# Kernel optimization log

Hardware: AMD Instinct MI355X
Metric: run time of the kernel (lower is better)

Reference implementation:

```python
import jax, jax.numpy as jnp
import numpy as np

N = 100000   # nodes
E = 3200000  # edges
G = 64       # graphs in batch
F_IN = 128   # num_features
H = 8        # hidden per TAGConv (hard-coded in module)
K = 3        # TAGConv hops (PyG default)
L = 3        # num_layers


def setup_inputs() -> dict:
    key = jax.random.key(0)
    ks = jax.random.split(key, 8)
    x = jax.random.normal(ks[0], (N, F_IN), dtype=jnp.float32)
    edge_index = jax.random.randint(ks[1], (2, E), 0, N, dtype=jnp.int32)
    batch = jnp.sort(jax.random.randint(ks[2], (N,), 0, G, dtype=jnp.int32))
    edge_weight = jax.random.uniform(ks[3], (E,), dtype=jnp.float32)
    W1 = jax.random.normal(ks[4], ((K + 1) * F_IN, H), dtype=jnp.float32) * 0.05
    W2 = jax.random.normal(ks[5], ((K + 1) * H, H), dtype=jnp.float32) * 0.1
    W3 = jax.random.normal(ks[6], ((K + 1) * H, H), dtype=jnp.float32) * 0.1
    fcW = jax.random.normal(ks[7], (2 * L * H, 2), dtype=jnp.float32) * 0.1
    return {
        'x': x, 'edge_index': edge_index, 'batch': batch,
        'edge_weight': edge_weight,
        'W1': W1, 'b1': jnp.zeros((H,), jnp.float32),
        'W2': W2, 'b2': jnp.zeros((H,), jnp.float32),
        'W3': W3, 'b3': jnp.zeros((H,), jnp.float32),
        'fcW': fcW, 'fcb': jnp.zeros((2,), jnp.float32),
    }


def _tag_conv(h, src, dst, norm, W, b):
    # TAGConv: concat [h, T h, T^2 h, T^3 h] then one linear (== sum of per-hop linears)
    xs = [h]
    for _ in range(K):
        h = jax.ops.segment_sum(h[src] * norm[:, None], dst, num_segments=N)
        xs.append(h)
    return jnp.concatenate(xs, axis=-1) @ W + b


def reference(x, edge_index, batch, edge_weight, W1, b1, W2, b2, W3, b3, fcW, fcb):
    src, dst = edge_index[0], edge_index[1]
    # GCN symmetric normalization, no self loops (PyG TAGConv default)
    deg = jax.ops.segment_sum(edge_weight, dst, num_segments=N)
    safe = jnp.where(deg > 0, deg, 1.0)
    dis = jnp.where(deg > 0, jax.lax.rsqrt(safe), 0.0)
    norm = dis[src] * edge_weight * dis[dst]  # [E]

    h = jax.nn.relu(_tag_conv(x, src, dst, norm, W1, b1))
    xs = [h]
    for (W, b) in ((W2, b2), (W3, b3)):
        h = jax.nn.relu(_tag_conv(h, src, dst, norm, W, b))
        xs.append(h)
    jk = jnp.concatenate(xs, axis=-1)  # [N, L*H] = [N, 24]

    # global max pool + global mean pool per graph
    gmax = jax.ops.segment_max(jk, batch, num_segments=G)
    gmax = jnp.where(jnp.isfinite(gmax), gmax, 0.0)
    gsum = jax.ops.segment_sum(jk, batch, num_segments=G)
    cnt = jax.ops.segment_sum(jnp.ones((N,), jk.dtype), batch, num_segments=G)
    gmean = gsum / jnp.maximum(cnt, 1.0)[:, None]
    pooled = jnp.concatenate([gmax, gmean], axis=-1)  # [G, 48]
    return pooled @ fcW + fcb  # [G, 2]
```

## Files before the change

kernel.cpp:

```cpp
#include <hip/hip_runtime.h>

static inline int div_up(int a, int b){ return (a + b - 1) / b; }

constexpr int FIN = 128;
constexpr unsigned long long DEG_MASK = ((unsigned long long)1 << 48) - 1;


__global__ __launch_bounds__(256) void count_deg_k(const int* __restrict__ dst,
    const float* __restrict__ w, unsigned long long* __restrict__ packed,
    unsigned short* __restrict__ ie, int E)
{
    int e = blockIdx.x * 256 + threadIdx.x;
    if (e >= E) return;
    int d = dst[e];
    unsigned long long add = ((unsigned long long)1 << 48)
                           | (unsigned long long)(w[e] * 4294967296.0f);
    unsigned long long old = atomicAdd(&packed[d], add);
    ie[e] = (unsigned short)(old >> 48);
}

__global__ __launch_bounds__(256) void scan_sum_k(const unsigned long long* __restrict__ packed,
    int* __restrict__ bsum, int n)
{
    __shared__ int lds[256];
    int t = threadIdx.x;
    int base = blockIdx.x * 1024 + t * 4;
    int s = 0;
    #pragma unroll
    for (int i = 0; i < 4; ++i) if (base + i < n) s += (int)(packed[base + i] >> 48);
    lds[t] = s; __syncthreads();
    for (int o = 128; o > 0; o >>= 1){
        if (t < o) lds[t] += lds[t + o];
        __syncthreads();
    }
    if (t == 0) bsum[blockIdx.x] = lds[0];
}

__global__ __launch_bounds__(256) void scan_block_k(int* __restrict__ bsum, int nb,
    int* __restrict__ rowptr, int n, int Etot)
{
    __shared__ int lds[256];
    int t = threadIdx.x;
    int v = (t < nb) ? bsum[t] : 0;
    lds[t] = v; __syncthreads();
    for (int o = 1; o < 256; o <<= 1){
        int add = (t >= o) ? lds[t - o] : 0;
        __syncthreads();
        lds[t] += add;
        __syncthreads();
    }
    if (t < nb) bsum[t] = lds[t] - v;
    if (t == 0) rowptr[n] = Etot;
}

__global__ __launch_bounds__(256) void scan_apply_k(const unsigned long long* __restrict__ packed,
    const int* __restrict__ bsum, int* __restrict__ rowptr, float* __restrict__ dis, int n)
{
    __shared__ int lds[256];
    int t = threadIdx.x;
    int base = blockIdx.x * 1024 + t * 4;
    int v[4]; int ts = 0;
    unsigned long long pk[4];
    #pragma unroll
    for (int i = 0; i < 4; ++i){
        pk[i] = (base + i < n) ? packed[base + i] : 0ull;
        v[i] = (int)(pk[i] >> 48); ts += v[i];
    }
    lds[t] = ts; __syncthreads();
    for (int o = 1; o < 256; o <<= 1){
        int add = (t >= o) ? lds[t - o] : 0;
        __syncthreads();
        lds[t] += add;
        __syncthreads();
    }
    int pre = lds[t] - ts + bsum[blockIdx.x];
    #pragma unroll
    for (int i = 0; i < 4; ++i){
        if (base + i < n){
            rowptr[base + i] = pre;
            float d = (float)(pk[i] & DEG_MASK) * (1.0f / 4294967296.0f);
            dis[base + i] = d > 0.f ? rsqrtf(d) : 0.f;
        }
        pre += v[i];
    }
}

__global__ __launch_bounds__(256) void scatter_k(const int* __restrict__ src,
    const int* __restrict__ dst, const float* __restrict__ w,
    const float* __restrict__ dis, const int* __restrict__ rowptr,
    const unsigned short* __restrict__ ie, int2* __restrict__ edges, int E)
{
    int e = blockIdx.x * 256 + threadIdx.x;
    if (e >= E) return;
    int s = src[e], d = dst[e];
    float nm = dis[s] * w[e] * dis[d];
    int pos = rowptr[d] + (int)ie[e];
    edges[pos] = make_int2(s, __float_as_int(nm));
}


__global__ __launch_bounds__(256) void gemm1_k(const float* __restrict__ x,
    const float* __restrict__ W, float* __restrict__ z, int n)
{
    int node = blockIdx.x * 256 + threadIdx.x;
    if (node >= n) return;
    const float4* xr = (const float4*)(x + (size_t)node * FIN);
    float acc[32];
    #pragma unroll
    for (int o = 0; o < 32; ++o) acc[o] = 0.f;
    #pragma unroll 2
    for (int fc = 0; fc < FIN / 4; ++fc){
        float4 xv = xr[fc];
        #pragma unroll
        for (int jj = 0; jj < 4; ++jj){
            float xs = jj == 0 ? xv.x : jj == 1 ? xv.y : jj == 2 ? xv.z : xv.w;
            int f = fc * 4 + jj;
            #pragma unroll
            for (int k = 0; k < 4; ++k)
                #pragma unroll
                for (int h = 0; h < 8; ++h)
                    acc[k * 8 + h] = fmaf(xs, W[((size_t)(k * FIN + f)) * 8 + h], acc[k * 8 + h]);
        }
    }
    float4* zr = (float4*)(z + (size_t)node * 32);
    #pragma unroll
    for (int q = 0; q < 8; ++q)
        zr[q] = make_float4(acc[q*4+0], acc[q*4+1], acc[q*4+2], acc[q*4+3]);
}

__global__ __launch_bounds__(256) void gemm_small_k(const float* __restrict__ hin,
    const float* __restrict__ W, float* __restrict__ z, int n)
{
    int node = blockIdx.x * 256 + threadIdx.x;
    if (node >= n) return;
    const float4* hr = (const float4*)(hin + (size_t)node * 8);
    float4 p0 = hr[0], p1 = hr[1];
    float hv[8] = {p0.x, p0.y, p0.z, p0.w, p1.x, p1.y, p1.z, p1.w};
    float acc[32];
    #pragma unroll
    for (int o = 0; o < 32; ++o) acc[o] = 0.f;
    #pragma unroll
    for (int f = 0; f < 8; ++f)
        #pragma unroll
        for (int k = 0; k < 4; ++k)
            #pragma unroll
            for (int h = 0; h < 8; ++h)
                acc[k * 8 + h] = fmaf(hv[f], W[(k * 8 + f) * 8 + h], acc[k * 8 + h]);
    float4* zr = (float4*)(z + (size_t)node * 32);
    #pragma unroll
    for (int q = 0; q < 8; ++q)
        zr[q] = make_float4(acc[q*4+0], acc[q*4+1], acc[q*4+2], acc[q*4+3]);
}


template<bool RELU, bool GEMM>
__global__ __launch_bounds__(256) void prop_k(const int2* __restrict__ edges,
    const int* __restrict__ rowptr, const float* __restrict__ uin, int instride,
    const float* __restrict__ addv, const float* __restrict__ bias,
    float* __restrict__ uout, const float* __restrict__ Wn, float* __restrict__ zout, int n)
{
    int t = blockIdx.x * 256 + threadIdx.x;
    int node = t >> 3, g = t & 7;
    if (node >= n) return;
    int r0 = rowptr[node], r1 = rowptr[node + 1];
    float acc = 0.f;
    int j = r0;
    for (; j + 4 <= r1; j += 4){
        int2 e0 = edges[j], e1 = edges[j+1], e2 = edges[j+2], e3 = edges[j+3];
        float a0 = uin[(size_t)e0.x * instride + g];
        float a1 = uin[(size_t)e1.x * instride + g];
        float a2 = uin[(size_t)e2.x * instride + g];
        float a3 = uin[(size_t)e3.x * instride + g];
        acc = fmaf(__int_as_float(e0.y), a0, acc);
        acc = fmaf(__int_as_float(e1.y), a1, acc);
        acc = fmaf(__int_as_float(e2.y), a2, acc);
        acc = fmaf(__int_as_float(e3.y), a3, acc);
    }
    for (; j < r1; ++j){
        int2 e0 = edges[j];
        acc = fmaf(__int_as_float(e0.y), uin[(size_t)e0.x * instride + g], acc);
    }
    float v = addv[(size_t)node * 32 + g] + acc;
    if (RELU) v = fmaxf(v + bias[g], 0.f);
    uout[(size_t)node * 8 + g] = v;
    if (GEMM){
        int lane = threadIdx.x & 63;
        int gbase = lane & ~7;
        float hrow[8];
        #pragma unroll
        for (int f = 0; f < 8; ++f) hrow[f] = __shfl(v, gbase + f);
        float zv[4];
        #pragma unroll
        for (int q = 0; q < 4; ++q){
            int o = g * 4 + q;
            int k = o >> 3, h = o & 7;
            float s = 0.f;
            #pragma unroll
            for (int f = 0; f < 8; ++f)
                s = fmaf(hrow[f], Wn[(k * 8 + f) * 8 + h], s);
            zv[q] = s;
        }
        *(float4*)(zout + (size_t)node * 32 + g * 4) = make_float4(zv[0], zv[1], zv[2], zv[3]);
    }
}


__global__ __launch_bounds__(256) void pool_k(const float* __restrict__ h1,
    const float* __restrict__ h2, const float* __restrict__ h3,
    const int* __restrict__ batch, unsigned* __restrict__ gmaxb,
    float* __restrict__ gsum, int* __restrict__ gcnt, int n)
{
    int t = blockIdx.x * 256 + threadIdx.x;
    int lane = threadIdx.x & 63;
    bool valid = (t < n);
    int b = valid ? batch[t] : -1;
    float v[24];
    #pragma unroll
    for (int q = 0; q < 24; ++q) v[q] = 0.f;
    if (valid){
        const float4* p1 = (const float4*)(h1 + (size_t)t * 8);
        const float4* p2 = (const float4*)(h2 + (size_t)t * 8);
        const float4* p3 = (const float4*)(h3 + (size_t)t * 8);
        float4 a0 = p1[0], a1 = p1[1], c0 = p2[0], c1 = p2[1], d0 = p3[0], d1 = p3[1];
        v[0]=a0.x; v[1]=a0.y; v[2]=a0.z; v[3]=a0.w; v[4]=a1.x; v[5]=a1.y; v[6]=a1.z; v[7]=a1.w;
        v[8]=c0.x; v[9]=c0.y; v[10]=c0.z; v[11]=c0.w; v[12]=c1.x; v[13]=c1.y; v[14]=c1.z; v[15]=c1.w;
        v[16]=d0.x; v[17]=d0.y; v[18]=d0.z; v[19]=d0.w; v[20]=d1.x; v[21]=d1.y; v[22]=d1.z; v[23]=d1.w;
    }
    int bl0 = __shfl(b, 0);
    bool uni = __all(b == bl0);
    if (uni){
        if (bl0 >= 0){
            #pragma unroll
            for (int q = 0; q < 24; ++q){
                float s = v[q], m = v[q];
                #pragma unroll
                for (int o = 1; o < 64; o <<= 1){
                    s += __shfl_xor(s, o);
                    m = fmaxf(m, __shfl_xor(m, o));
                }
                if (lane == 0){
                    atomicAdd(&gsum[bl0 * 24 + q], s);
                    atomicMax(&gmaxb[bl0 * 24 + q], __float_as_uint(m));
                }
            }
            if (lane == 0) atomicAdd(&gcnt[bl0], 64);
        }
    } else if (valid){
        #pragma unroll
        for (int q = 0; q < 24; ++q){
            atomicAdd(&gsum[b * 24 + q], v[q]);
            atomicMax(&gmaxb[b * 24 + q], __float_as_uint(v[q]));
        }
        atomicAdd(&gcnt[b], 1);
    }
}

__global__ __launch_bounds__(64) void fc_k(const unsigned* __restrict__ gmaxb,
    const float* __restrict__ gsum, const int* __restrict__ gcnt,
    const float* __restrict__ fcW, const float* __restrict__ fcb,
    float* __restrict__ out, int G)
{
    int g = threadIdx.x;
    if (g >= G) return;
    float pooled[48];
    #pragma unroll
    for (int q = 0; q < 24; ++q) pooled[q] = __uint_as_float(gmaxb[g * 24 + q]);
    float c = (float)gcnt[g];
    if (c < 1.f) c = 1.f;
    float inv = 1.f / c;
    #pragma unroll
    for (int q = 0; q < 24; ++q) pooled[24 + q] = gsum[g * 24 + q] * inv;
    float o0 = fcb[0], o1 = fcb[1];
    #pragma unroll
    for (int j = 0; j < 48; ++j){
        o0 = fmaf(pooled[j], fcW[j * 2 + 0], o0);
        o1 = fmaf(pooled[j], fcW[j * 2 + 1], o1);
    }
    out[g * 2 + 0] = o0;
    out[g * 2 + 1] = o1;
}


extern "C" void kernel_launch(void* const* d_in, const int* in_sizes, int n_in,
                              void* d_out, int out_size, void* d_ws, size_t ws_size,
                              hipStream_t stream)
{
    const float* x    = (const float*)d_in[0];
    const int*   ei   = (const int*)d_in[1];
    const int*   batch= (const int*)d_in[2];
    const float* w    = (const float*)d_in[3];
    const float* W1   = (const float*)d_in[4];
    const float* b1   = (const float*)d_in[5];
    const float* W2   = (const float*)d_in[6];
    const float* b2   = (const float*)d_in[7];
    const float* W3   = (const float*)d_in[8];
    const float* b3   = (const float*)d_in[9];
    const float* fcW  = (const float*)d_in[10];
    const float* fcb  = (const float*)d_in[11];
    float* out = (float*)d_out;

    const int N = in_sizes[2];
    const int E = in_sizes[3];
    const int G = out_size / 2;
    const int* src = ei;
    const int* dst = ei + E;

    char* base = (char*)d_ws;
    size_t off = 0;
    auto alloc = [&](size_t bytes) -> char* {
        char* r = base + off;
        off += (bytes + 255) & ~(size_t)255;
        return r;
    };
    unsigned long long* packed = (unsigned long long*)alloc((size_t)N * 8);
    unsigned* gmaxb  = (unsigned*)alloc((size_t)G * 24 * 4);
    float*    gsum   = (float*)   alloc((size_t)G * 24 * 4);
    int*      gcnt   = (int*)     alloc((size_t)G * 4);
    size_t zero_bytes = off;
    float*    dis    = (float*)   alloc((size_t)N * 4);
    unsigned short* ie = (unsigned short*)alloc((size_t)E * 2);
    int*      rowptr = (int*)     alloc((size_t)(N + 1) * 4);
    int*      bsum   = (int*)     alloc(256 * 4);
    int2*     edges  = (int2*)    alloc((size_t)E * 8);
    float*    zA     = (float*)   alloc((size_t)N * 32 * 4);
    float*    u0     = (float*)   alloc((size_t)N * 8 * 4);
    float*    u1     = (float*)   alloc((size_t)N * 8 * 4);
    float*    h1     = (float*)   alloc((size_t)N * 8 * 4);
    float*    h2     = (float*)   alloc((size_t)N * 8 * 4);
    float*    h3     = (float*)   alloc((size_t)N * 8 * 4);
    float*    zB     = (float*)   alloc((size_t)N * 32 * 4);
    bool fused = (off <= ws_size);
    if (!fused) zB = zA;

    hipMemsetAsync(d_ws, 0, zero_bytes, stream);

    dim3 blk(256);
    count_deg_k<<<div_up(E, 256), blk, 0, stream>>>(dst, w, packed, ie, E);
    int nb = div_up(N, 1024);
    scan_sum_k  <<<nb, blk, 0, stream>>>(packed, bsum, N);
    scan_block_k<<<1,  blk, 0, stream>>>(bsum, nb, rowptr, N, E);
    scan_apply_k<<<nb, blk, 0, stream>>>(packed, bsum, rowptr, dis, N);
    scatter_k<<<div_up(E, 256), blk, 0, stream>>>(src, dst, w, dis, rowptr, ie, edges, E);

    gemm1_k<<<div_up(N, 256), blk, 0, stream>>>(x, W1, zA, N);

    int pb = div_up(N * 8, 256);
    prop_k<false,false><<<pb, blk, 0, stream>>>(edges, rowptr, zA + 24, 32, zA + 16, nullptr, u0, nullptr, nullptr, N);
    prop_k<false,false><<<pb, blk, 0, stream>>>(edges, rowptr, u0, 8, zA + 8, nullptr, u1, nullptr, nullptr, N);
    if (fused){
        prop_k<true,true ><<<pb, blk, 0, stream>>>(edges, rowptr, u1, 8, zA, b1, h1, W2, zB, N);
    } else {
        prop_k<true,false><<<pb, blk, 0, stream>>>(edges, rowptr, u1, 8, zA, b1, h1, nullptr, nullptr, N);
        gemm_small_k<<<div_up(N, 256), blk, 0, stream>>>(h1, W2, zB, N);
    }
    prop_k<false,false><<<pb, blk, 0, stream>>>(edges, rowptr, zB + 24, 32, zB + 16, nullptr, u0, nullptr, nullptr, N);
    prop_k<false,false><<<pb, blk, 0, stream>>>(edges, rowptr, u0, 8, zB + 8, nullptr, u1, nullptr, nullptr, N);
    if (fused){
        prop_k<true,true ><<<pb, blk, 0, stream>>>(edges, rowptr, u1, 8, zB, b2, h2, W3, zA, N);
    } else {
        prop_k<true,false><<<pb, blk, 0, stream>>>(edges, rowptr, u1, 8, zB, b2, h2, nullptr, nullptr, N);
        gemm_small_k<<<div_up(N, 256), blk, 0, stream>>>(h2, W3, zA, N);
    }
    prop_k<false,false><<<pb, blk, 0, stream>>>(edges, rowptr, zA + 24, 32, zA + 16, nullptr, u0, nullptr, nullptr, N);
    prop_k<false,false><<<pb, blk, 0, stream>>>(edges, rowptr, u0, 8, zA + 8, nullptr, u1, nullptr, nullptr, N);
    prop_k<true,false><<<pb, blk, 0, stream>>>(edges, rowptr, u1, 8, zA, b3, h3, nullptr, nullptr, N);

    pool_k<<<div_up(N, 256), blk, 0, stream>>>(h1, h2, h3, batch, gmaxb, gsum, gcnt, N);
    fc_k<<<1, 64, 0, stream>>>(gmaxb, gsum, gcnt, fcW, fcb, out, G);
}
```

Measured before the change: 860.3 us.

## Split per-hop projections into separate arrays and fuse gemm1 into degree counting

Measured after the change: 772.1 us. 1.11x faster.

```diff
diff --git a/kernel.cpp b/kernel.cpp
--- a/kernel.cpp
+++ b/kernel.cpp
@@ -6,17 +6,50 @@
 constexpr unsigned long long DEG_MASK = ((unsigned long long)1 << 48) - 1;
 
 
-__global__ __launch_bounds__(256) void count_deg_k(const int* __restrict__ dst,
-    const float* __restrict__ w, unsigned long long* __restrict__ packed,
-    unsigned short* __restrict__ ie, int E)
-{
-    int e = blockIdx.x * 256 + threadIdx.x;
-    if (e >= E) return;
-    int d = dst[e];
-    unsigned long long add = ((unsigned long long)1 << 48)
-                           | (unsigned long long)(w[e] * 4294967296.0f);
-    unsigned long long old = atomicAdd(&packed[d], add);
-    ie[e] = (unsigned short)(old >> 48);
+__global__ __launch_bounds__(256) void count_gemm1_k(
+    const int* __restrict__ dst, const float* __restrict__ w,
+    unsigned long long* __restrict__ packed, unsigned short* __restrict__ ie, int E, int Eb,
+    const float* __restrict__ x, const float* __restrict__ W,
+    float* __restrict__ z0, float* __restrict__ z1,
+    float* __restrict__ z2, float* __restrict__ z3, int n)
+{
+    if (blockIdx.x < (unsigned)Eb){
+        int e = blockIdx.x * 256 + threadIdx.x;
+        if (e >= E) return;
+        int d = dst[e];
+        unsigned long long add = ((unsigned long long)1 << 48)
+                               | (unsigned long long)(w[e] * 4294967296.0f);
+        unsigned long long old = atomicAdd(&packed[d], add);
+        ie[e] = (unsigned short)(old >> 48);
+    } else {
+        int node = (blockIdx.x - Eb) * 256 + threadIdx.x;
+        if (node >= n) return;
+        const float4* xr = (const float4*)(x + (size_t)node * FIN);
+        float acc[32];
+        #pragma unroll
+        for (int o = 0; o < 32; ++o) acc[o] = 0.f;
+        #pragma unroll 2
+        for (int fc = 0; fc < FIN / 4; ++fc){
+            float4 xv = xr[fc];
+            #pragma unroll
+            for (int jj = 0; jj < 4; ++jj){
+                float xs = jj == 0 ? xv.x : jj == 1 ? xv.y : jj == 2 ? xv.z : xv.w;
+                int f = fc * 4 + jj;
+                #pragma unroll
+                for (int k = 0; k < 4; ++k)
+                    #pragma unroll
+                    for (int h = 0; h < 8; ++h)
+                        acc[k * 8 + h] = fmaf(xs, W[((size_t)(k * FIN + f)) * 8 + h], acc[k * 8 + h]);
+            }
+        }
+        float* zp[4] = {z0, z1, z2, z3};
+        #pragma unroll
+        for (int k = 0; k < 4; ++k){
+            float4* zr = (float4*)(zp[k] + (size_t)node * 8);
+            zr[0] = make_float4(acc[k*8+0], acc[k*8+1], acc[k*8+2], acc[k*8+3]);
+            zr[1] = make_float4(acc[k*8+4], acc[k*8+5], acc[k*8+6], acc[k*8+7]);
+        }
+    }
 }
 
 __global__ __launch_bounds__(256) void scan_sum_k(const unsigned long long* __restrict__ packed,
@@ -99,37 +132,9 @@
 }
 
 
-__global__ __launch_bounds__(256) void gemm1_k(const float* __restrict__ x,
-    const float* __restrict__ W, float* __restrict__ z, int n)
-{
-    int node = blockIdx.x * 256 + threadIdx.x;
-    if (node >= n) return;
-    const float4* xr = (const float4*)(x + (size_t)node * FIN);
-    float acc[32];
-    #pragma unroll
-    for (int o = 0; o < 32; ++o) acc[o] = 0.f;
-    #pragma unroll 2
-    for (int fc = 0; fc < FIN / 4; ++fc){
-        float4 xv = xr[fc];
-        #pragma unroll
-        for (int jj = 0; jj < 4; ++jj){
-            float xs = jj == 0 ? xv.x : jj == 1 ? xv.y : jj == 2 ? xv.z : xv.w;
-            int f = fc * 4 + jj;
-            #pragma unroll
-            for (int k = 0; k < 4; ++k)
-                #pragma unroll
-                for (int h = 0; h < 8; ++h)
-                    acc[k * 8 + h] = fmaf(xs, W[((size_t)(k * FIN + f)) * 8 + h], acc[k * 8 + h]);
-        }
-    }
-    float4* zr = (float4*)(z + (size_t)node * 32);
-    #pragma unroll
-    for (int q = 0; q < 8; ++q)
-        zr[q] = make_float4(acc[q*4+0], acc[q*4+1], acc[q*4+2], acc[q*4+3]);
-}
-
 __global__ __launch_bounds__(256) void gemm_small_k(const float* __restrict__ hin,
-    const float* __restrict__ W, float* __restrict__ z, int n)
+    const float* __restrict__ W, float* __restrict__ z0, float* __restrict__ z1,
+    float* __restrict__ z2, float* __restrict__ z3, int n)
 {
     int node = blockIdx.x * 256 + threadIdx.x;
     if (node >= n) return;
@@ -146,18 +151,23 @@
             #pragma unroll
             for (int h = 0; h < 8; ++h)
                 acc[k * 8 + h] = fmaf(hv[f], W[(k * 8 + f) * 8 + h], acc[k * 8 + h]);
-    float4* zr = (float4*)(z + (size_t)node * 32);
-    #pragma unroll
-    for (int q = 0; q < 8; ++q)
-        zr[q] = make_float4(acc[q*4+0], acc[q*4+1], acc[q*4+2], acc[q*4+3]);
+    float* zp[4] = {z0, z1, z2, z3};
+    #pragma unroll
+    for (int k = 0; k < 4; ++k){
+        float4* zr = (float4*)(zp[k] + (size_t)node * 8);
+        zr[0] = make_float4(acc[k*8+0], acc[k*8+1], acc[k*8+2], acc[k*8+3]);
+        zr[1] = make_float4(acc[k*8+4], acc[k*8+5], acc[k*8+6], acc[k*8+7]);
+    }
 }
 
 
 template<bool RELU, bool GEMM>
 __global__ __launch_bounds__(256) void prop_k(const int2* __restrict__ edges,
-    const int* __restrict__ rowptr, const float* __restrict__ uin, int instride,
+    const int* __restrict__ rowptr, const float* __restrict__ uin,
     const float* __restrict__ addv, const float* __restrict__ bias,
-    float* __restrict__ uout, const float* __restrict__ Wn, float* __restrict__ zout, int n)
+    float* __restrict__ uout, const float* __restrict__ Wn,
+    float* __restrict__ zo0, float* __restrict__ zo1,
+    float* __restrict__ zo2, float* __restrict__ zo3, int n)
 {
     int t = blockIdx.x * 256 + threadIdx.x;
     int node = t >> 3, g = t & 7;
@@ -167,10 +177,10 @@
     int j = r0;
     for (; j + 4 <= r1; j += 4){
         int2 e0 = edges[j], e1 = edges[j+1], e2 = edges[j+2], e3 = edges[j+3];
-        float a0 = uin[(size_t)e0.x * instride + g];
-        float a1 = uin[(size_t)e1.x * instride + g];
-        float a2 = uin[(size_t)e2.x * instride + g];
-        float a3 = uin[(size_t)e3.x * instride + g];
+        float a0 = uin[(size_t)e0.x * 8 + g];
+        float a1 = uin[(size_t)e1.x * 8 + g];
+        float a2 = uin[(size_t)e2.x * 8 + g];
+        float a3 = uin[(size_t)e3.x * 8 + g];
         acc = fmaf(__int_as_float(e0.y), a0, acc);
         acc = fmaf(__int_as_float(e1.y), a1, acc);
         acc = fmaf(__int_as_float(e2.y), a2, acc);
@@ -178,9 +188,9 @@
     }
     for (; j < r1; ++j){
         int2 e0 = edges[j];
-        acc = fmaf(__int_as_float(e0.y), uin[(size_t)e0.x * instride + g], acc);
-    }
-    float v = addv[(size_t)node * 32 + g] + acc;
+        acc = fmaf(__int_as_float(e0.y), uin[(size_t)e0.x * 8 + g], acc);
+    }
+    float v = addv[(size_t)node * 8 + g] + acc;
     if (RELU) v = fmaxf(v + bias[g], 0.f);
     uout[(size_t)node * 8 + g] = v;
     if (GEMM){
@@ -189,18 +199,19 @@
         float hrow[8];
         #pragma unroll
         for (int f = 0; f < 8; ++f) hrow[f] = __shfl(v, gbase + f);
+        int k = g >> 1;
         float zv[4];
         #pragma unroll
         for (int q = 0; q < 4; ++q){
-            int o = g * 4 + q;
-            int k = o >> 3, h = o & 7;
+            int h = (g & 1) * 4 + q;
             float s = 0.f;
             #pragma unroll
             for (int f = 0; f < 8; ++f)
                 s = fmaf(hrow[f], Wn[(k * 8 + f) * 8 + h], s);
             zv[q] = s;
         }
-        *(float4*)(zout + (size_t)node * 32 + g * 4) = make_float4(zv[0], zv[1], zv[2], zv[3]);
+        float* zp = (k == 0) ? zo0 : (k == 1) ? zo1 : (k == 2) ? zo2 : zo3;
+        *(float4*)(zp + (size_t)node * 8 + (g & 1) * 4) = make_float4(zv[0], zv[1], zv[2], zv[3]);
     }
 }
 
@@ -322,48 +333,49 @@
     int*      rowptr = (int*)     alloc((size_t)(N + 1) * 4);
     int*      bsum   = (int*)     alloc(256 * 4);
     int2*     edges  = (int2*)    alloc((size_t)E * 8);
-    float*    zA     = (float*)   alloc((size_t)N * 32 * 4);
+    float*    zA[4], *zB[4];
+    for (int k = 0; k < 4; ++k) zA[k] = (float*)alloc((size_t)N * 8 * 4);
     float*    u0     = (float*)   alloc((size_t)N * 8 * 4);
     float*    u1     = (float*)   alloc((size_t)N * 8 * 4);
     float*    h1     = (float*)   alloc((size_t)N * 8 * 4);
     float*    h2     = (float*)   alloc((size_t)N * 8 * 4);
     float*    h3     = (float*)   alloc((size_t)N * 8 * 4);
-    float*    zB     = (float*)   alloc((size_t)N * 32 * 4);
+    for (int k = 0; k < 4; ++k) zB[k] = (float*)alloc((size_t)N * 8 * 4);
     bool fused = (off <= ws_size);
-    if (!fused) zB = zA;
+    if (!fused) for (int k = 0; k < 4; ++k) zB[k] = zA[k];
 
     hipMemsetAsync(d_ws, 0, zero_bytes, stream);
 
     dim3 blk(256);
-    count_deg_k<<<div_up(E, 256), blk, 0, stream>>>(dst, w, packed, ie, E);
+    int Eb = div_up(E, 256), Nb = div_up(N, 256);
+    count_gemm1_k<<<Eb + Nb, blk, 0, stream>>>(dst, w, packed, ie, E, Eb,
+                                               x, W1, zA[0], zA[1], zA[2], zA[3], N);
     int nb = div_up(N, 1024);
     scan_sum_k  <<<nb, blk, 0, stream>>>(packed, bsum, N);
     scan_block_k<<<1,  blk, 0, stream>>>(bsum, nb, rowptr, N, E);
     scan_apply_k<<<nb, blk, 0, stream>>>(packed, bsum, rowptr, dis, N);
     scatter_k<<<div_up(E, 256), blk, 0, stream>>>(src, dst, w, dis, rowptr, ie, edges, E);
 
-    gemm1_k<<<div_up(N, 256), blk, 0, stream>>>(x, W1, zA, N);
-
     int pb = div_up(N * 8, 256);
-    prop_k<false,false><<<pb, blk, 0, stream>>>(edges, rowptr, zA + 24, 32, zA + 16, nullptr, u0, nullptr, nullptr, N);
-    prop_k<false,false><<<pb, blk, 0, stream>>>(edges, rowptr, u0, 8, zA + 8, nullptr, u1, nullptr, nullptr, N);
+    prop_k<false,false><<<pb, blk, 0, stream>>>(edges, rowptr, zA[3], zA[2], nullptr, u0, nullptr, nullptr, nullptr, nullptr, nullptr, N);
+    prop_k<false,false><<<pb, blk, 0, stream>>>(edges, rowptr, u0, zA[1], nullptr, u1, nullptr, nullptr, nullptr, nullptr, nullptr, N);
     if (fused){
-        prop_k<true,true ><<<pb, blk, 0, stream>>>(edges, rowptr, u1, 8, zA, b1, h1, W2, zB, N);
+        prop_k<true,true ><<<pb, blk, 0, stream>>>(edges, rowptr, u1, zA[0], b1, h1, W2, zB[0], zB[1], zB[2], zB[3], N);
     } else {
-        prop_k<true,false><<<pb, blk, 0, stream>>>(edges, rowptr, u1, 8, zA, b1, h1, nullptr, nullptr, N);
-        gemm_small_k<<<div_up(N, 256), blk, 0, stream>>>(h1, W2, zB, N);
-    }
-    prop_k<false,false><<<pb, blk, 0, stream>>>(edges, rowptr, zB + 24, 32, zB + 16, nullptr, u0, nullptr, nullptr, N);
-    prop_k<false,false><<<pb, blk, 0, stream>>>(edges, rowptr, u0, 8, zB + 8, nullptr, u1, nullptr, nullptr, N);
+        prop_k<true,false><<<pb, blk, 0, stream>>>(edges, rowptr, u1, zA[0], b1, h1, nullptr, nullptr, nullptr, nullptr, nullptr, N);
+        gemm_small_k<<<div_up(N, 256), blk, 0, stream>>>(h1, W2, zB[0], zB[1], zB[2], zB[3], N);
+    }
+    prop_k<false,false><<<pb, blk, 0, stream>>>(edges, rowptr, zB[3], zB[2], nullptr, u0, nullptr, nullptr, nullptr, nullptr, nullptr, N);
+    prop_k<false,false><<<pb, blk, 0, stream>>>(edges, rowptr, u0, zB[1], nullptr, u1, nullptr, nullptr, nullptr, nullptr, nullptr, N);
     if (fused){
-        prop_k<true,true ><<<pb, blk, 0, stream>>>(edges, rowptr, u1, 8, zB, b2, h2, W3, zA, N);
+        prop_k<true,true ><<<pb, blk, 0, stream>>>(edges, rowptr, u1, zB[0], b2, h2, W3, zA[0], zA[1], zA[2], zA[3], N);
     } else {
-        prop_k<true,false><<<pb, blk, 0, stream>>>(edges, rowptr, u1, 8, zB, b2, h2, nullptr, nullptr, N);
-        gemm_small_k<<<div_up(N, 256), blk, 0, stream>>>(h2, W3, zA, N);
-    }
-    prop_k<false,false><<<pb, blk, 0, stream>>>(edges, rowptr, zA + 24, 32, zA + 16, nullptr, u0, nullptr, nullptr, N);
-    prop_k<false,false><<<pb, blk, 0, stream>>>(edges, rowptr, u0, 8, zA + 8, nullptr, u1, nullptr, nullptr, N);
-    prop_k<true,false><<<pb, blk, 0, stream>>>(edges, rowptr, u1, 8, zA, b3, h3, nullptr, nullptr, N);
+        prop_k<true,false><<<pb, blk, 0, stream>>>(edges, rowptr, u1, zB[0], b2, h2, nullptr, nullptr, nullptr, nullptr, nullptr, N);
+        gemm_small_k<<<div_up(N, 256), blk, 0, stream>>>(h2, W3, zA[0], zA[1], zA[2], zA[3], N);
+    }
+    prop_k<false,false><<<pb, blk, 0, stream>>>(edges, rowptr, zA[3], zA[2], nullptr, u0, nullptr, nullptr, nullptr, nullptr, nullptr, N);
+    prop_k<false,false><<<pb, blk, 0, stream>>>(edges, rowptr, u0, zA[1], nullptr, u1, nullptr, nullptr, nullptr, nullptr, nullptr, N);
+    prop_k<true,false><<<pb, blk, 0, stream>>>(edges, rowptr, u1, zA[0], b3, h3, nullptr, nullptr, nullptr, nullptr, nullptr, N);
 
     pool_k<<<div_up(N, 256), blk, 0, stream>>>(h1, h2, h3, batch, gmaxb, gsum, gcnt, N);
     fc_k<<<1, 64, 0, stream>>>(gmaxb, gsum, gcnt, fcW, fcb, out, G);
```
